# Performance work log

Measured on AMD Instinct MI355X. Metric: run time of the kernel, lower is better.

The kernel has to match this reference:

```python
import jax, jax.numpy as jnp
import numpy as np

_DIMS = [("fu1",2,2),("fu2",2,2),("ku1",4,4),("ku2",4,4),("hu1",6,6),("hu2",6,6),("md1",11,16),("md2",16,16),("md3",16,6),("hd1",6,4),("hd2",4,4),("kd1",4,2),("kd2",2,2),("ha1",8,4),("ha2",4,1),("ka1",6,4),("ka2",4,1),("fa1",4,4),("fa2",4,1)]


def setup_inputs() -> dict:
    key = jax.random.key(0)
    B = 2_000_000
    inp = {"x": jax.random.normal(key, (B, 11), dtype=jnp.float32)}
    for i, (name, din, dout) in enumerate(_DIMS):
        kw = jax.random.fold_in(key, i + 1)
        scale = float(np.sqrt(6.0 / (din + dout)))  # xavier_uniform gain=1
        inp[name + "_w"] = jax.random.uniform(kw, (din, dout), jnp.float32, -scale, scale)
        inp[name + "_b"] = jnp.zeros((dout,), jnp.float32)  # nn.Linear default bias ~ small; zeros for determinism
    return inp


def _lin(x, w, b):
    # weights stored as (in, out) == torch W.T
    return x @ w + b


def reference(x, fu1_w, fu1_b, fu2_w, fu2_b, ku1_w, ku1_b, ku2_w, ku2_b, hu1_w, hu1_b, hu2_w, hu2_b, md1_w, md1_b, md2_w, md2_b, md3_w, md3_b, hd1_w, hd1_b, hd2_w, hd2_b, kd1_w, kd1_b, kd2_w, kd2_b, ha1_w, ha1_b, ha2_w, ha2_b, ka1_w, ka1_b, ka2_w, ka2_b, fa1_w, fa1_b, fa2_w, fa2_b):
    r = jax.nn.relu
    h = x[:, 2:3]; k = x[:, 3:4]; f = x[:, 4:5]
    hd = x[:, 8:9]; kd = x[:, 9:10]; fd = x[:, 10:11]
    m_obs = x[:, jnp.array([0, 1, 5, 6, 7])]  # [B,5]
    f_up = r(_lin(r(_lin(jnp.concatenate([f, fd], 1), fu1_w, fu1_b)), fu2_w, fu2_b))            # [B,2]
    k_up = r(_lin(r(_lin(jnp.concatenate([k, kd, f_up], 1), ku1_w, ku1_b)), ku2_w, ku2_b))      # [B,4]
    h_up = r(_lin(r(_lin(jnp.concatenate([h, hd, k_up], 1), hu1_w, hu1_b)), hu2_w, hu2_b))      # [B,6]
    m_in = jnp.concatenate([m_obs, h_up], 1)                                                    # [B,11]
    m_down = r(_lin(r(_lin(r(_lin(m_in, md1_w, md1_b)), md2_w, md2_b)), md3_w, md3_b))          # [B,6]
    h_down = r(_lin(r(_lin(m_down, hd1_w, hd1_b)), hd2_w, hd2_b))                               # [B,4]
    k_down = r(_lin(r(_lin(h_down, kd1_w, kd1_b)), kd2_w, kd2_b))                               # [B,2]
    h_act = _lin(r(_lin(jnp.concatenate([h, hd, m_down], 1), ha1_w, ha1_b)), ha2_w, ha2_b)      # [B,1]
    k_act = _lin(r(_lin(jnp.concatenate([k, kd, h_down], 1), ka1_w, ka1_b)), ka2_w, ka2_b)      # [B,1]
    f_act = _lin(r(_lin(jnp.concatenate([f, fd, k_down], 1), fa1_w, fa1_b)), fa2_w, fa2_b)      # [B,1]
    return jnp.concatenate([h_act, f_act, k_act], 1)                                            # [B,3]
```

## Files before the change

kernel.cpp:

```cpp
#include <hip/hip_runtime.h>

#define BLOCK 256
#define R 4

struct WPtrs {
    const float* w[19];
    const float* b[19];
};

enum LId {FU1,FU2,KU1,KU2,HU1,HU2,MD1,MD2,MD3,HD1,HD2,KD1,KD2,HA1,HA2,KA1,KA2,FA1,FA2};

template<int DIN,int DOUT,bool RELU>
__device__ __forceinline__ void lin(const float (&in)[R][DIN], float (&out)[R][DOUT],
                                    const float* __restrict__ w, const float* __restrict__ b) {
#pragma unroll
    for (int j = 0; j < DOUT; ++j) {
        const float bj = b[j];
        float acc[R];
#pragma unroll
        for (int r = 0; r < R; ++r) acc[r] = bj;
#pragma unroll
        for (int i = 0; i < DIN; ++i) {
            const float wij = w[i*DOUT + j];
#pragma unroll
            for (int r = 0; r < R; ++r) acc[r] = __builtin_fmaf(in[r][i], wij, acc[r]);
        }
#pragma unroll
        for (int r = 0; r < R; ++r) out[r][j] = RELU ? fmaxf(acc[r], 0.0f) : acc[r];
    }
}

__global__ __launch_bounds__(BLOCK) void pnet_kernel(
    const float* __restrict__ x, float* __restrict__ out, int B, WPtrs P) {
    const long long t = (long long)blockIdx.x * BLOCK + threadIdx.x;
    const long long row0 = t * R;
    if (row0 >= B) return;
    const bool full = (row0 + R) <= B;

    float xin[R][11];
    if (full) {
        const float4* p = (const float4*)(x + row0 * 11);
        float4 v[11];
#pragma unroll
        for (int i = 0; i < 11; ++i) v[i] = p[i];
        const float* fv = (const float*)&v[0];
#pragma unroll
        for (int r = 0; r < R; ++r)
#pragma unroll
            for (int c = 0; c < 11; ++c) xin[r][c] = fv[r*11 + c];
    } else {
#pragma unroll
        for (int r = 0; r < R; ++r) {
            long long row = row0 + r; if (row > (long long)B - 1) row = B - 1;
#pragma unroll
            for (int c = 0; c < 11; ++c) xin[r][c] = x[row*11 + c];
        }
    }

    float fin[R][2], tf[R][2], f_up[R][2];
#pragma unroll
    for (int r = 0; r < R; ++r) { fin[r][0] = xin[r][4]; fin[r][1] = xin[r][10]; }
    lin<2,2,true>(fin, tf, P.w[FU1], P.b[FU1]);
    lin<2,2,true>(tf, f_up, P.w[FU2], P.b[FU2]);

    float kin[R][4], tk[R][4], k_up[R][4];
#pragma unroll
    for (int r = 0; r < R; ++r) {
        kin[r][0] = xin[r][3]; kin[r][1] = xin[r][9];
        kin[r][2] = f_up[r][0]; kin[r][3] = f_up[r][1];
    }
    lin<4,4,true>(kin, tk, P.w[KU1], P.b[KU1]);
    lin<4,4,true>(tk, k_up, P.w[KU2], P.b[KU2]);

    float hin[R][6], th[R][6], h_up[R][6];
#pragma unroll
    for (int r = 0; r < R; ++r) {
        hin[r][0] = xin[r][2]; hin[r][1] = xin[r][8];
#pragma unroll
        for (int i = 0; i < 4; ++i) hin[r][2+i] = k_up[r][i];
    }
    lin<6,6,true>(hin, th, P.w[HU1], P.b[HU1]);
    lin<6,6,true>(th, h_up, P.w[HU2], P.b[HU2]);

    float min_[R][11], t16a[R][16], t16b[R][16], m_down[R][6];
#pragma unroll
    for (int r = 0; r < R; ++r) {
        min_[r][0] = xin[r][0]; min_[r][1] = xin[r][1]; min_[r][2] = xin[r][5];
        min_[r][3] = xin[r][6]; min_[r][4] = xin[r][7];
#pragma unroll
        for (int i = 0; i < 6; ++i) min_[r][5+i] = h_up[r][i];
    }
    lin<11,16,true>(min_, t16a, P.w[MD1], P.b[MD1]);
    lin<16,16,true>(t16a, t16b, P.w[MD2], P.b[MD2]);
    lin<16,6,true>(t16b, m_down, P.w[MD3], P.b[MD3]);

    float t4b[R][4], h_down[R][4];
    lin<6,4,true>(m_down, t4b, P.w[HD1], P.b[HD1]);
    lin<4,4,true>(t4b, h_down, P.w[HD2], P.b[HD2]);

    float t2b[R][2], k_down[R][2];
    lin<4,2,true>(h_down, t2b, P.w[KD1], P.b[KD1]);
    lin<2,2,true>(t2b, k_down, P.w[KD2], P.b[KD2]);

    float ha_in[R][8], t4c[R][4], h_act[R][1];
#pragma unroll
    for (int r = 0; r < R; ++r) {
        ha_in[r][0] = xin[r][2]; ha_in[r][1] = xin[r][8];
#pragma unroll
        for (int i = 0; i < 6; ++i) ha_in[r][2+i] = m_down[r][i];
    }
    lin<8,4,true>(ha_in, t4c, P.w[HA1], P.b[HA1]);
    lin<4,1,false>(t4c, h_act, P.w[HA2], P.b[HA2]);

    float ka_in[R][6], t4d[R][4], k_act[R][1];
#pragma unroll
    for (int r = 0; r < R; ++r) {
        ka_in[r][0] = xin[r][3]; ka_in[r][1] = xin[r][9];
#pragma unroll
        for (int i = 0; i < 4; ++i) ka_in[r][2+i] = h_down[r][i];
    }
    lin<6,4,true>(ka_in, t4d, P.w[KA1], P.b[KA1]);
    lin<4,1,false>(t4d, k_act, P.w[KA2], P.b[KA2]);

    float fa_in[R][4], t4e[R][4], f_act[R][1];
#pragma unroll
    for (int r = 0; r < R; ++r) {
        fa_in[r][0] = xin[r][4]; fa_in[r][1] = xin[r][10];
#pragma unroll
        for (int i = 0; i < 2; ++i) fa_in[r][2+i] = k_down[r][i];
    }
    lin<4,4,true>(fa_in, t4e, P.w[FA1], P.b[FA1]);
    lin<4,1,false>(t4e, f_act, P.w[FA2], P.b[FA2]);

    if (full) {
        float ob[12];
#pragma unroll
        for (int r = 0; r < R; ++r) {
            ob[r*3+0] = h_act[r][0];
            ob[r*3+1] = f_act[r][0];
            ob[r*3+2] = k_act[r][0];
        }
        float4* po = (float4*)(out + row0 * 3);
#pragma unroll
        for (int i = 0; i < 3; ++i) po[i] = ((const float4*)ob)[i];
    } else {
#pragma unroll
        for (int r = 0; r < R; ++r) {
            long long row = row0 + r;
            if (row < B) {
                out[row*3+0] = h_act[r][0];
                out[row*3+1] = f_act[r][0];
                out[row*3+2] = k_act[r][0];
            }
        }
    }
}

extern "C" void kernel_launch(void* const* d_in, const int* in_sizes, int n_in,
                              void* d_out, int out_size, void* d_ws, size_t ws_size,
                              hipStream_t stream) {
    const float* x = (const float*)d_in[0];
    float* out = (float*)d_out;
    const int B = in_sizes[0] / 11;

    WPtrs P;
    for (int i = 0; i < 19; ++i) {
        P.w[i] = (const float*)d_in[1 + 2*i];
        P.b[i] = (const float*)d_in[2 + 2*i];
    }

    const long long nthreads = ((long long)B + R - 1) / R;
    const int blocks = (int)((nthreads + BLOCK - 1) / BLOCK);
    pnet_kernel<<<blocks, BLOCK, 0, stream>>>(x, out, B, P);
}
```

Baseline: 253.6 us.

## Pack two rows per thread into float2 vectors for packed FMA math

Each thread now processes two rows instead of four. The per-row scalar arrays are replaced with 2-wide float vectors so the compiler can emit packed FP32 FMA and max instructions, and launching twice as many threads is meant to raise occupancy. Loads and stores switch from float4 to float2. The trade-off is narrower memory accesses and weight loads amortised over fewer rows per thread.

New measurement: 344.0 us. +35.6%, slower.

```diff
diff --git a/kernel.cpp b/kernel.cpp
--- a/kernel.cpp
+++ b/kernel.cpp
@@ -1,7 +1,8 @@
 #include <hip/hip_runtime.h>
 
 #define BLOCK 256
-#define R 4
+
+typedef float v2f __attribute__((ext_vector_type(2)));
 
 struct WPtrs {
     const float* w[19];
@@ -11,148 +12,104 @@
 enum LId {FU1,FU2,KU1,KU2,HU1,HU2,MD1,MD2,MD3,HD1,HD2,KD1,KD2,HA1,HA2,KA1,KA2,FA1,FA2};
 
 template<int DIN,int DOUT,bool RELU>
-__device__ __forceinline__ void lin(const float (&in)[R][DIN], float (&out)[R][DOUT],
+__device__ __forceinline__ void lin(const v2f (&in)[DIN], v2f (&out)[DOUT],
                                     const float* __restrict__ w, const float* __restrict__ b) {
 #pragma unroll
     for (int j = 0; j < DOUT; ++j) {
         const float bj = b[j];
-        float acc[R];
-#pragma unroll
-        for (int r = 0; r < R; ++r) acc[r] = bj;
+        v2f acc = {bj, bj};
 #pragma unroll
         for (int i = 0; i < DIN; ++i) {
             const float wij = w[i*DOUT + j];
-#pragma unroll
-            for (int r = 0; r < R; ++r) acc[r] = __builtin_fmaf(in[r][i], wij, acc[r]);
+            v2f wv = {wij, wij};
+            acc = __builtin_elementwise_fma(in[i], wv, acc);
         }
-#pragma unroll
-        for (int r = 0; r < R; ++r) out[r][j] = RELU ? fmaxf(acc[r], 0.0f) : acc[r];
+        if (RELU) {
+            v2f z = {0.0f, 0.0f};
+            out[j] = __builtin_elementwise_max(acc, z);
+        } else {
+            out[j] = acc;
+        }
     }
 }
 
 __global__ __launch_bounds__(BLOCK) void pnet_kernel(
     const float* __restrict__ x, float* __restrict__ out, int B, WPtrs P) {
     const long long t = (long long)blockIdx.x * BLOCK + threadIdx.x;
-    const long long row0 = t * R;
+    const long long row0 = t * 2;
     if (row0 >= B) return;
-    const bool full = (row0 + R) <= B;
+    const bool full = (row0 + 2) <= B;
 
-    float xin[R][11];
+    v2f xin[11];
     if (full) {
-        const float4* p = (const float4*)(x + row0 * 11);
-        float4 v[11];
+        const v2f* p = (const v2f*)(x + row0 * 11);
+        v2f v[11];
 #pragma unroll
         for (int i = 0; i < 11; ++i) v[i] = p[i];
         const float* fv = (const float*)&v[0];
 #pragma unroll
-        for (int r = 0; r < R; ++r)
+        for (int c = 0; c < 11; ++c) { xin[c].x = fv[c]; xin[c].y = fv[11 + c]; }
+    } else {
+        const float* pr = x + row0 * 11;
 #pragma unroll
-            for (int c = 0; c < 11; ++c) xin[r][c] = fv[r*11 + c];
-    } else {
-#pragma unroll
-        for (int r = 0; r < R; ++r) {
-            long long row = row0 + r; if (row > (long long)B - 1) row = B - 1;
-#pragma unroll
-            for (int c = 0; c < 11; ++c) xin[r][c] = x[row*11 + c];
-        }
+        for (int c = 0; c < 11; ++c) { xin[c].x = pr[c]; xin[c].y = pr[c]; }
     }
 
-    float fin[R][2], tf[R][2], f_up[R][2];
-#pragma unroll
-    for (int r = 0; r < R; ++r) { fin[r][0] = xin[r][4]; fin[r][1] = xin[r][10]; }
+    v2f fin[2] = {xin[4], xin[10]};
+    v2f tf[2], f_up[2];
     lin<2,2,true>(fin, tf, P.w[FU1], P.b[FU1]);
     lin<2,2,true>(tf, f_up, P.w[FU2], P.b[FU2]);
 
-    float kin[R][4], tk[R][4], k_up[R][4];
-#pragma unroll
-    for (int r = 0; r < R; ++r) {
-        kin[r][0] = xin[r][3]; kin[r][1] = xin[r][9];
-        kin[r][2] = f_up[r][0]; kin[r][3] = f_up[r][1];
-    }
+    v2f kin[4] = {xin[3], xin[9], f_up[0], f_up[1]};
+    v2f tk[4], k_up[4];
     lin<4,4,true>(kin, tk, P.w[KU1], P.b[KU1]);
     lin<4,4,true>(tk, k_up, P.w[KU2], P.b[KU2]);
 
-    float hin[R][6], th[R][6], h_up[R][6];
-#pragma unroll
-    for (int r = 0; r < R; ++r) {
-        hin[r][0] = xin[r][2]; hin[r][1] = xin[r][8];
-#pragma unroll
-        for (int i = 0; i < 4; ++i) hin[r][2+i] = k_up[r][i];
-    }
+    v2f hin[6] = {xin[2], xin[8], k_up[0], k_up[1], k_up[2], k_up[3]};
+    v2f th[6], h_up[6];
     lin<6,6,true>(hin, th, P.w[HU1], P.b[HU1]);
     lin<6,6,true>(th, h_up, P.w[HU2], P.b[HU2]);
 
-    float min_[R][11], t16a[R][16], t16b[R][16], m_down[R][6];
-#pragma unroll
-    for (int r = 0; r < R; ++r) {
-        min_[r][0] = xin[r][0]; min_[r][1] = xin[r][1]; min_[r][2] = xin[r][5];
-        min_[r][3] = xin[r][6]; min_[r][4] = xin[r][7];
-#pragma unroll
-        for (int i = 0; i < 6; ++i) min_[r][5+i] = h_up[r][i];
-    }
+    v2f min_[11] = {xin[0], xin[1], xin[5], xin[6], xin[7],
+                    h_up[0], h_up[1], h_up[2], h_up[3], h_up[4], h_up[5]};
+    v2f t16a[16], t16b[16], m_down[6];
     lin<11,16,true>(min_, t16a, P.w[MD1], P.b[MD1]);
     lin<16,16,true>(t16a, t16b, P.w[MD2], P.b[MD2]);
     lin<16,6,true>(t16b, m_down, P.w[MD3], P.b[MD3]);
 
-    float t4b[R][4], h_down[R][4];
+    v2f t4b[4], h_down[4];
     lin<6,4,true>(m_down, t4b, P.w[HD1], P.b[HD1]);
     lin<4,4,true>(t4b, h_down, P.w[HD2], P.b[HD2]);
 
-    float t2b[R][2], k_down[R][2];
+    v2f t2b[2], k_down[2];
     lin<4,2,true>(h_down, t2b, P.w[KD1], P.b[KD1]);
     lin<2,2,true>(t2b, k_down, P.w[KD2], P.b[KD2]);
 
-    float ha_in[R][8], t4c[R][4], h_act[R][1];
-#pragma unroll
-    for (int r = 0; r < R; ++r) {
-        ha_in[r][0] = xin[r][2]; ha_in[r][1] = xin[r][8];
-#pragma unroll
-        for (int i = 0; i < 6; ++i) ha_in[r][2+i] = m_down[r][i];
-    }
+    v2f ha_in[8] = {xin[2], xin[8], m_down[0], m_down[1], m_down[2], m_down[3], m_down[4], m_down[5]};
+    v2f t4c[4], h_act[1];
     lin<8,4,true>(ha_in, t4c, P.w[HA1], P.b[HA1]);
     lin<4,1,false>(t4c, h_act, P.w[HA2], P.b[HA2]);
 
-    float ka_in[R][6], t4d[R][4], k_act[R][1];
-#pragma unroll
-    for (int r = 0; r < R; ++r) {
-        ka_in[r][0] = xin[r][3]; ka_in[r][1] = xin[r][9];
-#pragma unroll
-        for (int i = 0; i < 4; ++i) ka_in[r][2+i] = h_down[r][i];
-    }
+    v2f ka_in[6] = {xin[3], xin[9], h_down[0], h_down[1], h_down[2], h_down[3]};
+    v2f t4d[4], k_act[1];
     lin<6,4,true>(ka_in, t4d, P.w[KA1], P.b[KA1]);
     lin<4,1,false>(t4d, k_act, P.w[KA2], P.b[KA2]);
 
-    float fa_in[R][4], t4e[R][4], f_act[R][1];
-#pragma unroll
-    for (int r = 0; r < R; ++r) {
-        fa_in[r][0] = xin[r][4]; fa_in[r][1] = xin[r][10];
-#pragma unroll
-        for (int i = 0; i < 2; ++i) fa_in[r][2+i] = k_down[r][i];
-    }
+    v2f fa_in[4] = {xin[4], xin[10], k_down[0], k_down[1]};
+    v2f t4e[4], f_act[1];
     lin<4,4,true>(fa_in, t4e, P.w[FA1], P.b[FA1]);
     lin<4,1,false>(t4e, f_act, P.w[FA2], P.b[FA2]);
 
     if (full) {
-        float ob[12];
+        float ob[6] = {h_act[0].x, f_act[0].x, k_act[0].x,
+                       h_act[0].y, f_act[0].y, k_act[0].y};
+        v2f* po = (v2f*)(out + row0 * 3);
 #pragma unroll
-        for (int r = 0; r < R; ++r) {
-            ob[r*3+0] = h_act[r][0];
-            ob[r*3+1] = f_act[r][0];
-            ob[r*3+2] = k_act[r][0];
-        }
-        float4* po = (float4*)(out + row0 * 3);
-#pragma unroll
-        for (int i = 0; i < 3; ++i) po[i] = ((const float4*)ob)[i];
+        for (int i = 0; i < 3; ++i) po[i] = ((const v2f*)ob)[i];
     } else {
-#pragma unroll
-        for (int r = 0; r < R; ++r) {
-            long long row = row0 + r;
-            if (row < B) {
-                out[row*3+0] = h_act[r][0];
-                out[row*3+1] = f_act[r][0];
-                out[row*3+2] = k_act[r][0];
-            }
-        }
+        out[row0*3+0] = h_act[0].x;
+        out[row0*3+1] = f_act[0].x;
+        out[row0*3+2] = k_act[0].x;
     }
 }
 
@@ -169,7 +126,7 @@
         P.b[i] = (const float*)d_in[2 + 2*i];
     }
 
-    const long long nthreads = ((long long)B + R - 1) / R;
+    const long long nthreads = ((long long)B + 1) / 2;
     const int blocks = (int)((nthreads + BLOCK - 1) / BLOCK);
     pnet_kernel<<<blocks, BLOCK, 0, stream>>>(x, out, B, P);
 }
```
